# Kernel optimization log

Hardware: AMD Instinct MI355X
Metric: run time of the kernel (lower is better)

Reference implementation:

```python
import jax, jax.numpy as jnp
import numpy as np

N = 8192
DISCO_LAMBDA = 0.1
DCORR_POWER = 2  # static, from __init__


def setup_inputs() -> dict:
    key = jax.random.key(0)
    k1, k2, k3, k4 = jax.random.split(key, 4)
    inferences = jax.random.uniform(k1, (N,), dtype=jnp.float32, minval=1e-6, maxval=1.0 - 1e-6)
    labels = jax.random.randint(k2, (N,), 0, 2, dtype=jnp.int32)
    disco_target = jax.random.normal(k3, (N,), dtype=jnp.float32)
    weights = jax.random.uniform(k4, (N,), dtype=jnp.float32)
    return {"inferences": inferences, "labels": labels,
            "disco_target": disco_target, "weights": weights}


def _bce(p, y, w):
    # torch F.binary_cross_entropy: clamps log terms at -100, mean reduction
    logp = jnp.clip(jnp.log(p), -100.0)
    log1mp = jnp.clip(jnp.log1p(-p), -100.0)
    return jnp.mean(w * -(y * logp + (1.0 - y) * log1mp))


def _dcorr(v1, v2, w, mask):
    # mask selects labels==0 subset; zero weights + divide by subset count
    # reproduces torch means over the fancy-indexed subset exactly.
    nf = jnp.sum(mask)                      # subset size (traced scalar)
    wm = w * mask                           # [N]
    amat = jnp.abs(v1[:, None] - v1[None, :])   # [N,N]
    bmat = jnp.abs(v2[:, None] - v2[None, :])   # [N,N]
    a_row = (amat @ wm) / nf                # weighted row means
    b_row = (bmat @ wm) / nf
    a_tot = jnp.dot(a_row, wm) / nf
    b_tot = jnp.dot(b_row, wm) / nf
    Amat = amat - a_row[None, :] - a_row[:, None] + a_tot  # double-centered
    Bmat = bmat - b_row[None, :] - b_row[:, None] + b_tot
    AB = jnp.dot((Amat * Bmat) @ wm, wm) / (nf * nf)
    AA = jnp.dot((Amat * Amat) @ wm, wm) / (nf * nf)
    BB = jnp.dot((Bmat * Bmat) @ wm, wm) / (nf * nf)
    if DCORR_POWER == 1:
        return AB / jnp.sqrt(AA * BB)
    elif DCORR_POWER == 2:
        return AB ** 2 / (AA * BB)
    else:
        return (AB / jnp.sqrt(AA * BB)) ** DCORR_POWER


def reference(inferences, labels, disco_target, weights):
    y = labels.astype(inferences.dtype)
    bce = _bce(inferences, y, weights)
    mask = (labels == 0).astype(inferences.dtype)
    dcorr = _dcorr(inferences, disco_target, weights, mask)
    total = bce + DISCO_LAMBDA * dcorr
    return (total, bce, DISCO_LAMBDA * dcorr)
```

## Files before the change

kernel.cpp:

```cpp
#include <hip/hip_runtime.h>
#include <math.h>

constexpr int N_ELEM = 8192;
constexpr int BLK    = 256;
constexpr int WAVES_PER_BLK = 4;
constexpr int ROWS_PER_WAVE = 2;
constexpr int ROWS_PER_BLK  = WAVES_PER_BLK * ROWS_PER_WAVE;
constexpr int KP_GRID = N_ELEM / ROWS_PER_BLK;
constexpr int BLKF    = 1024;
constexpr float LAMBDA = 0.1f;


__global__ void __launch_bounds__(BLK) kp_pairs(
        const float* __restrict__ inf, const int* __restrict__ lab,
        const float* __restrict__ tgt, const float* __restrict__ wt,
        double* __restrict__ gpart) {
    __shared__ double sred[WAVES_PER_BLK][6];
    int tx = threadIdx.x, lane = tx & 63, wid = tx >> 6;
    int r0 = blockIdx.x * ROWS_PER_BLK + wid * ROWS_PER_WAVE;

    float x0 = inf[r0],     y0 = tgt[r0];
    float x1 = inf[r0 + 1], y1 = tgt[r0 + 1];
    float u0 = (lab[r0]     == 0) ? wt[r0]     : 0.0f;
    float u1 = (lab[r0 + 1] == 0) ? wt[r0 + 1] : 0.0f;

    float ra0 = 0.f, rb0 = 0.f, pp0 = 0.f;
    float ra1 = 0.f, rb1 = 0.f, pp1 = 0.f;
#pragma unroll 4
    for (int jj = 0; jj < N_ELEM / 64; ++jj) {
        int j = jj * 64 + lane;
        float xj = inf[j], yj = tgt[j], wj = wt[j];
        int   lj = lab[j];
        float u = (lj == 0) ? wj : 0.0f;
        float d0 = x0 - xj, e0 = y0 - yj;
        ra0 = fmaf(u, fabsf(d0), ra0);
        rb0 = fmaf(u, fabsf(e0), rb0);
        pp0 = fmaf(u, fabsf(d0) * fabsf(e0), pp0);
        float d1 = x1 - xj, e1 = y1 - yj;
        ra1 = fmaf(u, fabsf(d1), ra1);
        rb1 = fmaf(u, fabsf(e1), rb1);
        pp1 = fmaf(u, fabsf(d1) * fabsf(e1), pp1);
    }
#pragma unroll
    for (int d = 32; d > 0; d >>= 1) {
        ra0 += __shfl_xor(ra0, d); rb0 += __shfl_xor(rb0, d); pp0 += __shfl_xor(pp0, d);
        ra1 += __shfl_xor(ra1, d); rb1 += __shfl_xor(rb1, d); pp1 += __shfl_xor(pp1, d);
    }
    if (lane == 0) {
        double U0 = (double)u0, U1 = (double)u1;
        double A0 = (double)ra0, B0 = (double)rb0, P0 = (double)pp0;
        double A1 = (double)ra1, B1 = (double)rb1, P1 = (double)pp1;
        sred[wid][0] = U0 * P0 + U1 * P1;
        sred[wid][1] = U0 * A0 + U1 * A1;
        sred[wid][2] = U0 * A0 * A0 + U1 * A1 * A1;
        sred[wid][3] = U0 * B0 + U1 * B1;
        sred[wid][4] = U0 * B0 * B0 + U1 * B1 * B1;
        sred[wid][5] = U0 * A0 * B0 + U1 * A1 * B1;
    }
    __syncthreads();
    if (tx == 0) {
        double* g = gpart + (size_t)blockIdx.x * 6;
#pragma unroll
        for (int k = 0; k < 6; ++k)
            g[k] = sred[0][k] + sred[1][k] + sred[2][k] + sred[3][k];
    }
}

__global__ void __launch_bounds__(BLKF) kf_final(
        const float* __restrict__ inf, const int* __restrict__ lab,
        const float* __restrict__ tgt, const float* __restrict__ wt,
        const double* __restrict__ gpart, float* __restrict__ out) {
    __shared__ float  redM[BLKF / 64][8];
    __shared__ double redG[BLKF / 64][6];
    int tx = threadIdx.x, lane = tx & 63, wid = tx >> 6;

    float vb = 0.f, vn = 0.f, vw = 0.f, v1a = 0.f, v2a = 0.f, v1b = 0.f, v2b = 0.f;
#pragma unroll
    for (int k = 0; k < N_ELEM / BLKF; ++k) {
        int i = k * BLKF + tx;
        float p = inf[i];
        int   y = lab[i];
        float w = wt[i];
        float t = tgt[i];
        float logp   = fmaxf(logf(p),    -100.0f);
        float log1mp = fmaxf(log1pf(-p), -100.0f);
        float yf = (float)y;
        vb += w * -(yf * logp + (1.0f - yf) * log1mp);
        bool  m  = (y == 0);
        float mf = m ? 1.0f : 0.0f;
        float wm = m ? w : 0.0f;
        vn += mf; vw += wm;
        v1a += wm * p; v2a += wm * p * p;
        v1b += wm * t; v2b += wm * t * t;
    }
    float vm[7] = {vb, vn, vw, v1a, v2a, v1b, v2b};
#pragma unroll
    for (int k = 0; k < 7; ++k) {
        float s = vm[k];
#pragma unroll
        for (int d = 32; d > 0; d >>= 1) s += __shfl_xor(s, d);
        if (lane == 0) redM[wid][k] = s;
    }

    double a0, a1, a2, a3, a4, a5;
    {
        const double* g = gpart + (size_t)tx * 6;
        a0 = g[0]; a1 = g[1]; a2 = g[2]; a3 = g[3]; a4 = g[4]; a5 = g[5];
    }
#pragma unroll
    for (int d = 32; d > 0; d >>= 1) {
        a0 += __shfl_xor(a0, d); a1 += __shfl_xor(a1, d); a2 += __shfl_xor(a2, d);
        a3 += __shfl_xor(a3, d); a4 += __shfl_xor(a4, d); a5 += __shfl_xor(a5, d);
    }
    if (lane == 0) {
        redG[wid][0] = a0; redG[wid][1] = a1; redG[wid][2] = a2;
        redG[wid][3] = a3; redG[wid][4] = a4; redG[wid][5] = a5;
    }
    __syncthreads();

    if (tx == 0) {
        double M[7] = {0, 0, 0, 0, 0, 0, 0};
        double G[6] = {0, 0, 0, 0, 0, 0};
        for (int wv = 0; wv < BLKF / 64; ++wv) {
#pragma unroll
            for (int k = 0; k < 7; ++k) M[k] += (double)redM[wv][k];
#pragma unroll
            for (int k = 0; k < 6; ++k) G[k] += redG[wv][k];
        }
        double bceS = M[0], NF = M[1], W = M[2];
        double S1a = M[3], S2a = M[4], S1b = M[5], S2b = M[6];
        double P = G[0], Ra1 = G[1], Ra2 = G[2], Rb1 = G[3], Rb2 = G[4], Rab = G[5];

        double in1 = 1.0 / NF;
        double in2 = in1 * in1, in3 = in2 * in1, in4 = in2 * in2;

        double AAa = 2.0 * (W * S2a - S1a * S1a)
                   - 4.0 * Ra2 * in1 + 2.0 * W * Ra2 * in2
                   + 4.0 * Ra1 * Ra1 * in2 - 4.0 * W * Ra1 * Ra1 * in3
                   + W * W * Ra1 * Ra1 * in4;
        double BBa = 2.0 * (W * S2b - S1b * S1b)
                   - 4.0 * Rb2 * in1 + 2.0 * W * Rb2 * in2
                   + 4.0 * Rb1 * Rb1 * in2 - 4.0 * W * Rb1 * Rb1 * in3
                   + W * W * Rb1 * Rb1 * in4;
        double ABa = P
                   - 4.0 * Rab * in1 + 2.0 * W * Rab * in2
                   + 4.0 * Ra1 * Rb1 * in2 - 4.0 * W * Ra1 * Rb1 * in3
                   + W * W * Ra1 * Rb1 * in4;

        double AB = ABa * in2, AA = AAa * in2, BB = BBa * in2;
        double dcorr = (AB * AB) / (AA * BB);
        double ld = (double)LAMBDA * dcorr;
        double bce = bceS / (double)N_ELEM;
        out[0] = (float)(bce + ld);
        out[1] = (float)bce;
        out[2] = (float)ld;
    }
}

extern "C" void kernel_launch(void* const* d_in, const int* in_sizes, int n_in,
                              void* d_out, int out_size, void* d_ws, size_t ws_size,
                              hipStream_t stream) {
    const float* inf = (const float*)d_in[0];
    const int*   lab = (const int*)d_in[1];
    const float* tgt = (const float*)d_in[2];
    const float* wt  = (const float*)d_in[3];
    float* out = (float*)d_out;
    double* gpart = (double*)d_ws;

    kp_pairs<<<KP_GRID, BLK, 0, stream>>>(inf, lab, tgt, wt, gpart);
    kf_final<<<1, BLKF, 0, stream>>>(inf, lab, tgt, wt, gpart, out);
}
```

Measured before the change: 92.71 us.

## Stage column data in double-buffered LDS tiles and process four rows per wave

The pairwise kernel now packs each column's value, target and masked weight into a float4 and stages it in double-buffered shared-memory chunks, prefetching the next chunk from global memory during compute. Each wave handles four rows instead of two, which halves the grid and amortizes every column load over more rows. The final kernel guards its partial-sum reads against the smaller grid. The cost is more registers per thread and a block-wide barrier per chunk.

```diff
diff --git a/kernel.cpp b/kernel.cpp
--- a/kernel.cpp
+++ b/kernel.cpp
@@ -3,11 +3,13 @@
 
 constexpr int N_ELEM = 8192;
 constexpr int BLK    = 256;
-constexpr int WAVES_PER_BLK = 4;
-constexpr int ROWS_PER_WAVE = 2;
-constexpr int ROWS_PER_BLK  = WAVES_PER_BLK * ROWS_PER_WAVE;
-constexpr int KP_GRID = N_ELEM / ROWS_PER_BLK;
-constexpr int BLKF    = 1024;
+constexpr int WAVES  = 4;
+constexpr int RPW    = 4;
+constexpr int RPB    = WAVES * RPW;
+constexpr int KP_GRID = N_ELEM / RPB;
+constexpr int CHUNK  = 512;
+constexpr int NCHUNK = N_ELEM / CHUNK;
+constexpr int BLKF   = 1024;
 constexpr float LAMBDA = 0.1f;
 
 
@@ -15,47 +17,77 @@
         const float* __restrict__ inf, const int* __restrict__ lab,
         const float* __restrict__ tgt, const float* __restrict__ wt,
         double* __restrict__ gpart) {
-    __shared__ double sred[WAVES_PER_BLK][6];
-    int tx = threadIdx.x, lane = tx & 63, wid = tx >> 6;
-    int r0 = blockIdx.x * ROWS_PER_BLK + wid * ROWS_PER_WAVE;
-
-    float x0 = inf[r0],     y0 = tgt[r0];
-    float x1 = inf[r0 + 1], y1 = tgt[r0 + 1];
-    float u0 = (lab[r0]     == 0) ? wt[r0]     : 0.0f;
-    float u1 = (lab[r0 + 1] == 0) ? wt[r0 + 1] : 0.0f;
-
-    float ra0 = 0.f, rb0 = 0.f, pp0 = 0.f;
-    float ra1 = 0.f, rb1 = 0.f, pp1 = 0.f;
-#pragma unroll 4
-    for (int jj = 0; jj < N_ELEM / 64; ++jj) {
-        int j = jj * 64 + lane;
-        float xj = inf[j], yj = tgt[j], wj = wt[j];
-        int   lj = lab[j];
-        float u = (lj == 0) ? wj : 0.0f;
-        float d0 = x0 - xj, e0 = y0 - yj;
-        ra0 = fmaf(u, fabsf(d0), ra0);
-        rb0 = fmaf(u, fabsf(e0), rb0);
-        pp0 = fmaf(u, fabsf(d0) * fabsf(e0), pp0);
-        float d1 = x1 - xj, e1 = y1 - yj;
-        ra1 = fmaf(u, fabsf(d1), ra1);
-        rb1 = fmaf(u, fabsf(e1), rb1);
-        pp1 = fmaf(u, fabsf(d1) * fabsf(e1), pp1);
-    }
-#pragma unroll
-    for (int d = 32; d > 0; d >>= 1) {
-        ra0 += __shfl_xor(ra0, d); rb0 += __shfl_xor(rb0, d); pp0 += __shfl_xor(pp0, d);
-        ra1 += __shfl_xor(ra1, d); rb1 += __shfl_xor(rb1, d); pp1 += __shfl_xor(pp1, d);
+    __shared__ float4 sc[2][CHUNK];
+    __shared__ double sred[WAVES][6];
+    const int tx = threadIdx.x, lane = tx & 63, wid = tx >> 6;
+    const int r0 = blockIdx.x * RPB + wid * RPW;
+
+    float x[RPW], y[RPW], u[RPW];
+#pragma unroll
+    for (int r = 0; r < RPW; ++r) {
+        x[r] = inf[r0 + r];
+        y[r] = tgt[r0 + r];
+        u[r] = (lab[r0 + r] == 0) ? wt[r0 + r] : 0.0f;
+    }
+    float ra[RPW] = {}, rb[RPW] = {}, pp[RPW] = {};
+
+#pragma unroll
+    for (int s = 0; s < CHUNK / BLK; ++s) {
+        int j = s * BLK + tx;
+        float wmj = (lab[j] == 0) ? wt[j] : 0.0f;
+        sc[0][j] = make_float4(inf[j], tgt[j], wmj, 0.0f);
+    }
+    __syncthreads();
+
+    for (int ch = 0; ch < NCHUNK; ++ch) {
+        const int cur = ch & 1;
+        const int chn = (ch + 1) & (NCHUNK - 1);
+        const int jb  = chn * CHUNK + tx;
+        float p0n = inf[jb],       t0n = tgt[jb],       w0n = wt[jb];
+        float p1n = inf[jb + BLK], t1n = tgt[jb + BLK], w1n = wt[jb + BLK];
+        int   l0n = lab[jb],       l1n = lab[jb + BLK];
+
+#pragma unroll
+        for (int s = 0; s < CHUNK / 64; ++s) {
+            float4 cj = sc[cur][s * 64 + lane];
+#pragma unroll
+            for (int r = 0; r < RPW; ++r) {
+                float fa = fabsf(x[r] - cj.x);
+                float fb = fabsf(y[r] - cj.y);
+                ra[r] = fmaf(cj.z, fa, ra[r]);
+                rb[r] = fmaf(cj.z, fb, rb[r]);
+                pp[r] = fmaf(cj.z, fa * fb, pp[r]);
+            }
+        }
+        if (ch + 1 < NCHUNK) {
+            sc[cur ^ 1][tx]       = make_float4(p0n, t0n, (l0n == 0) ? w0n : 0.0f, 0.0f);
+            sc[cur ^ 1][BLK + tx] = make_float4(p1n, t1n, (l1n == 0) ? w1n : 0.0f, 0.0f);
+        }
+        __syncthreads();
+    }
+
+#pragma unroll
+    for (int r = 0; r < RPW; ++r) {
+#pragma unroll
+        for (int d = 32; d > 0; d >>= 1) {
+            ra[r] += __shfl_xor(ra[r], d);
+            rb[r] += __shfl_xor(rb[r], d);
+            pp[r] += __shfl_xor(pp[r], d);
+        }
     }
     if (lane == 0) {
-        double U0 = (double)u0, U1 = (double)u1;
-        double A0 = (double)ra0, B0 = (double)rb0, P0 = (double)pp0;
-        double A1 = (double)ra1, B1 = (double)rb1, P1 = (double)pp1;
-        sred[wid][0] = U0 * P0 + U1 * P1;
-        sred[wid][1] = U0 * A0 + U1 * A1;
-        sred[wid][2] = U0 * A0 * A0 + U1 * A1 * A1;
-        sred[wid][3] = U0 * B0 + U1 * B1;
-        sred[wid][4] = U0 * B0 * B0 + U1 * B1 * B1;
-        sred[wid][5] = U0 * A0 * B0 + U1 * A1 * B1;
+        double s0 = 0, s1 = 0, s2 = 0, s3 = 0, s4 = 0, s5 = 0;
+#pragma unroll
+        for (int r = 0; r < RPW; ++r) {
+            double U = (double)u[r];
+            double A = (double)ra[r], B = (double)rb[r], Pp = (double)pp[r];
+            s0 += U * Pp;
+            s1 += U * A;  s2 += U * A * A;
+            s3 += U * B;  s4 += U * B * B;
+            s5 += U * A * B;
+        }
+        sred[wid][0] = s0; sred[wid][1] = s1; sred[wid][2] = s2;
+        sred[wid][3] = s3; sred[wid][4] = s4; sred[wid][5] = s5;
     }
     __syncthreads();
     if (tx == 0) {
@@ -102,8 +134,8 @@
         if (lane == 0) redM[wid][k] = s;
     }
 
-    double a0, a1, a2, a3, a4, a5;
-    {
+    double a0 = 0, a1 = 0, a2 = 0, a3 = 0, a4 = 0, a5 = 0;
+    if (tx < KP_GRID) {
         const double* g = gpart + (size_t)tx * 6;
         a0 = g[0]; a1 = g[1]; a2 = g[2]; a3 = g[3]; a4 = g[4]; a5 = g[5];
     }
```

Measured after the change: 87.97 us. 5.1% less time.
